# Kernel tuning notes

Hardware: AMD Instinct MI355X
Metric: run time of the kernel (lower is better)

## Reference

```python
import jax, jax.numpy as jnp
import numpy as np

EPS = 1e-8


def eq_linear(z, weight, bias):
    # EqualisedLinear: runtime weight scale c = 1/sqrt(in_features)
    c = 1.0 / np.sqrt(weight.shape[1]).astype(np.float32)
    return z @ (weight * c).T + bias


def mod_conv(x, w_raw, s, demodulate):
    # w_raw: [out, in, k, k], s: [b, in]
    out_c, in_c, k, _ = w_raw.shape
    c = 1.0 / np.sqrt(in_c * k * k).astype(np.float32)
    wt = w_raw * c
    # per-sample modulated weights: [b, out, in, k, k]
    ws = wt[None] * s[:, None, :, None, None]
    if demodulate:
        sigma_inv = jax.lax.rsqrt(jnp.sum(ws * ws, axis=(2, 3, 4), keepdims=True) + EPS)
        ws = ws * sigma_inv
    def conv1(xi, wi):
        return jax.lax.conv_general_dilated(
            xi[None], wi, window_strides=(1, 1), padding='SAME',
            dimension_numbers=('NCHW', 'OIHW', 'NCHW'))[0]
    return jax.vmap(conv1)(x, ws)


def lrelu(v):
    return jax.nn.leaky_relu(v, 0.2)


def style_block(x, w, noise, style_w, style_b, conv_w, noise_scale, bias):
    s = eq_linear(w, style_w, style_b)
    x = mod_conv(x, conv_w, s, demodulate=True)
    x = x + noise_scale[None, :, None, None] * noise
    return lrelu(x + bias[None, :, None, None])


def to_rgb(x, w, style_w, style_b, conv_w, bias):
    s = eq_linear(w, style_w, style_b)
    x = mod_conv(x, conv_w, s, demodulate=False)
    return lrelu(x + bias[None, :, None, None])


def setup_inputs() -> dict:
    key = jax.random.key(0)
    ks = jax.random.split(key, 16)
    B, C, H, W = 16, 512, 64, 64
    D = 512
    OUT = 3
    return {
        'x': jax.random.normal(ks[0], (B, C, H, W), jnp.float32),
        'w': jax.random.normal(ks[1], (B, D), jnp.float32),
        'noise1': jax.random.normal(ks[2], (B, 1, H, W), jnp.float32),
        'noise2': jax.random.normal(ks[3], (B, 1, H, W), jnp.float32),
        'sb1_style_w': jax.random.normal(ks[4], (C, D), jnp.float32),
        'sb1_style_b': jnp.ones((C,), jnp.float32),
        'sb1_conv_w': jax.random.normal(ks[5], (C, C, 3, 3), jnp.float32),
        'sb1_noise_scale': 0.1 * jax.random.normal(ks[6], (1,), jnp.float32),
        'sb1_bias': 0.1 * jax.random.normal(ks[7], (C,), jnp.float32),
        'sb2_style_w': jax.random.normal(ks[8], (C, D), jnp.float32),
        'sb2_style_b': jnp.ones((C,), jnp.float32),
        'sb2_conv_w': jax.random.normal(ks[9], (C, C, 3, 3), jnp.float32),
        'sb2_noise_scale': 0.1 * jax.random.normal(ks[10], (1,), jnp.float32),
        'sb2_bias': 0.1 * jax.random.normal(ks[11], (C,), jnp.float32),
        'rgb_style_w': jax.random.normal(ks[12], (C, D), jnp.float32),
        'rgb_style_b': jnp.ones((C,), jnp.float32),
        'rgb_conv_w': jax.random.normal(ks[13], (OUT, C, 1, 1), jnp.float32),
        'rgb_bias': 0.1 * jax.random.normal(ks[14], (OUT,), jnp.float32),
    }


def reference(x, w, noise1, noise2,
              sb1_style_w, sb1_style_b, sb1_conv_w, sb1_noise_scale, sb1_bias,
              sb2_style_w, sb2_style_b, sb2_conv_w, sb2_noise_scale, sb2_bias,
              rgb_style_w, rgb_style_b, rgb_conv_w, rgb_bias):
    x = style_block(x, w, noise1, sb1_style_w, sb1_style_b, sb1_conv_w, sb1_noise_scale, sb1_bias)
    x = style_block(x, w, noise2, sb2_style_w, sb2_style_b, sb2_conv_w, sb2_noise_scale, sb2_bias)
    rgb = to_rgb(x, w, rgb_style_w, rgb_style_b, rgb_conv_w, rgb_bias)
    return (x, rgb)
```

## Files before the change

### kernel.cpp

```cpp
#include <hip/hip_runtime.h>
#include <hip/hip_bf16.h>

typedef float f32x4 __attribute__((ext_vector_type(4)));
typedef short short8 __attribute__((ext_vector_type(8)));

#define CC    512
#define PIX   4096
#define ROWB  4224
#define TILE6 25344
#define TILE4 16896

__device__ __forceinline__ unsigned short f2bf(float f){
    __hip_bfloat16 h = __float2bfloat16(f);
    return __builtin_bit_cast(unsigned short, h);
}
__device__ __forceinline__ unsigned pk2(float a, float b){
    return (unsigned)f2bf(a) | ((unsigned)f2bf(b) << 16);
}
__device__ __forceinline__ void mfma_bf16(f32x4& c, short8 a, short8 b){
    asm("v_mfma_f32_16x16x32_bf16 %0, %1, %2, %0" : "+v"(c) : "v"(a), "v"(b));
}
__device__ __forceinline__ void gl_lds16(const void* g, void* l){
    __builtin_amdgcn_global_load_lds(
        (const __attribute__((address_space(1))) unsigned int*)g,
        (__attribute__((address_space(3))) unsigned int*)l, 16, 0, 0);
}

__global__ void k_style3(const float* __restrict__ w,
                         const float* __restrict__ sw0, const float* __restrict__ sb0, float* __restrict__ o0,
                         const float* __restrict__ sw1, const float* __restrict__ sb1, float* __restrict__ o1,
                         const float* __restrict__ sw2, const float* __restrict__ sb2, float* __restrict__ o2){
    __shared__ float wl[512];
    const int b = blockIdx.x, l = blockIdx.y, tid = threadIdx.x;
    const float* sw = (l==0) ? sw0 : (l==1 ? sw1 : sw2);
    const float* sb = (l==0) ? sb0 : (l==1 ? sb1 : sb2);
    float* so       = (l==0) ? o0  : (l==1 ? o1  : o2);
    wl[tid]       = w[b*512 + tid];
    wl[tid + 256] = w[b*512 + 256 + tid];
    __syncthreads();
    const float c = 0.044194173824159216f;
    for (int cc = tid; cc < 512; cc += 256){
        const float4* row = (const float4*)(sw + cc*512);
        float acc = 0.f;
        #pragma unroll 4
        for (int dd = 0; dd < 128; ++dd){
            float4 v = row[dd];
            float4 wv = ((const float4*)wl)[dd];
            acc += v.x*wv.x + v.y*wv.y + v.z*wv.z + v.w*wv.w;
        }
        so[b*512 + cc] = acc * c + sb[cc];
    }
}

__global__ void k_w2(const float* __restrict__ cw1, const float* __restrict__ cw2,
                     float* __restrict__ w2_1, float* __restrict__ w2_2){
    int gid = blockIdx.x*256 + threadIdx.x;
    int layer = gid >> 18; int r = gid & 262143;
    const float* cw = layer ? cw2 : cw1;
    float* w2 = layer ? w2_2 : w2_1;
    const float c2 = 1.0f/4608.0f;
    const float* p = cw + r*9;
    float sum = 0.f;
    #pragma unroll
    for (int t=0;t<9;++t){ float v = p[t]; sum += v*v; }
    w2[r] = sum * c2;
}

__global__ void k_demod2(const float* __restrict__ w21, const float* __restrict__ w22,
                         const float* __restrict__ s1,  const float* __restrict__ s2,
                         float* __restrict__ d1, float* __restrict__ d2){
    __shared__ float s2l[512];
    const int b = blockIdx.x, l = blockIdx.y, o = threadIdx.x;
    const float* w2 = l ? w22 : w21;
    const float* s  = l ? s2  : s1;
    float* d        = l ? d2  : d1;
    float sv = s[b*512 + o]; s2l[o] = sv*sv;
    __syncthreads();
    const float4* row = (const float4*)(w2 + o*512);
    const float4* sq  = (const float4*)s2l;
    float acc = 0.f;
    #pragma unroll 4
    for (int i=0;i<128;++i){
        float4 a = row[i], bq = sq[i];
        acc += a.x*bq.x + a.y*bq.y + a.z*bq.z + a.w*bq.w;
    }
    d[b*512 + o] = rsqrtf(acc + 1e-8f);
}

__global__ void k_pack(const float* __restrict__ cw1, const float* __restrict__ cw2,
                       uint4* __restrict__ wpk1, uint4* __restrict__ wpk2){
    int gid = blockIdx.x*256 + threadIdx.x;
    int layer = (gid >= 294912);
    int r = layer ? gid - 294912 : gid;
    const float* cw = layer ? cw2 : cw1;
    uint4* dst = layer ? wpk2 : wpk1;
    int lane = r & 63;
    int ofr  = (r>>6) & 31;
    int cb   = (r>>11) & 15;
    int t    = r>>15;
    int o  = ofr*16 + (lane&15);
    int i0 = cb*32 + (lane>>4)*8;
    const float c = 0.014731391274719738f;
    const float* src = cw + (o*512 + i0)*9 + t;
    float f[8];
    #pragma unroll
    for (int j=0;j<8;++j) f[j] = src[j*9]*c;
    uint4 wv;
    wv.x = pk2(f[0],f[1]); wv.y = pk2(f[2],f[3]);
    wv.z = pk2(f[4],f[5]); wv.w = pk2(f[6],f[7]);
    dst[r] = wv;
}

__global__ void k_stage_g(const float* __restrict__ x, const float* __restrict__ s,
                          char* __restrict__ xpg){
    __shared__ float s_lds[512];
    const int tid = threadIdx.x;
    const int rb = blockIdx.x, b = blockIdx.y;
    const int r0 = rb*4;
    s_lds[tid]       = s[b*512 + tid];
    s_lds[tid + 256] = s[b*512 + 256 + tid];
    __syncthreads();
    const int scol   = tid & 63;
    const int schunk = (tid>>6) & 3;
    unsigned wcol = (unsigned)((scol+1)*64 + schunk*16);
    wcol ^= (unsigned)((((scol+1)>>1)&3)<<4);
    const float* xb = x + (size_t)b * (512*PIX);
    for (int cb=0; cb<16; ++cb){
        char* dst = xpg + ((size_t)((b*16 + rb)*16 + cb))*TILE6;
        float sv[8];
        #pragma unroll
        for (int j=0;j<8;++j) sv[j] = s_lds[cb*32 + schunk*8 + j];
        const float* srcbase = xb + (size_t)(cb*32 + schunk*8)*PIX + scol;
        #pragma unroll
        for (int row=0; row<6; ++row){
            int gr = r0 - 1 + row;
            uint4 wq = make_uint4(0u,0u,0u,0u);
            if (0 <= gr && gr < 64){
                const float* sp = srcbase + gr*64;
                float f0 = sp[0*PIX]*sv[0], f1 = sp[1*PIX]*sv[1];
                float f2 = sp[2*PIX]*sv[2], f3 = sp[3*PIX]*sv[3];
                float f4 = sp[4*PIX]*sv[4], f5 = sp[5*PIX]*sv[5];
                float f6 = sp[6*PIX]*sv[6], f7 = sp[7*PIX]*sv[7];
                wq.x = pk2(f0,f1); wq.y = pk2(f2,f3);
                wq.z = pk2(f4,f5); wq.w = pk2(f6,f7);
            }
            *(uint4*)(dst + row*ROWB + wcol) = wq;
        }
        if (tid < 48){
            int row = tid>>3; int hc = (tid&4) ? 65 : 0; int ck = tid&3;
            unsigned a = (unsigned)((row*66 + hc)*64 + ck*16);
            a ^= (unsigned)(((hc>>1)&3)<<4);
            *(uint4*)(dst + a) = make_uint4(0u,0u,0u,0u);
        }
    }
}

__global__ __launch_bounds__(256, 2)
void k_conv(const char* __restrict__ xpg, float* __restrict__ y,
            const unsigned short* __restrict__ wpk,
            const float* __restrict__ dmod, const float* __restrict__ noise,
            const float* __restrict__ nsp, const float* __restrict__ bias){
    __shared__ __align__(16) char smem[2*TILE4];
    char* xh0 = smem;
    char* xh1 = smem + TILE4;

    const int tid  = threadIdx.x;
    const int obp  = blockIdx.x;
    const int rb   = blockIdx.y;
    const int b    = blockIdx.z;
    const int r0   = rb*2;
    const int lane = tid & 63;
    const int wv   = tid >> 6;
    const int ln15 = lane & 15;
    const int hi   = lane >> 4;

    f32x4 acc[4][8];
    #pragma unroll
    for (int mi=0;mi<4;++mi)
        #pragma unroll
        for (int ni=0;ni<8;++ni) acc[mi][ni] = (f32x4)(0.f);

    unsigned bcol[3][4];
    #pragma unroll
    for (int dxi=0; dxi<3; ++dxi)
        #pragma unroll
        for (int ni=0; ni<4; ++ni){
            int xcol = ni*16 + ln15 + dxi;
            unsigned a = (unsigned)(xcol*64 + hi*16);
            a ^= (unsigned)(((xcol>>1)&3)<<4);
            bcol[dxi][ni] = a;
        }

    const char* tbase = xpg + ((size_t)((b*16 + (rb>>1))*16))*TILE6
                            + (size_t)(rb&1)*2*ROWB;
    auto stage = [&](int cb2, char* dstb){
        const char* src = tbase + (size_t)cb2*TILE6;
        #pragma unroll
        for (int k=0;k<4;++k)
            gl_lds16(src + (size_t)(tid + k*256)*16, dstb + (tid + k*256)*16);
        if (tid < 32)
            gl_lds16(src + (size_t)(1024 + tid)*16, dstb + (1024 + tid)*16);
    };

    stage(0, xh0);

    const short8* wpf = (const short8*)wpk + (size_t)(obp*16 + wv*4)*64 + lane;

    #pragma unroll 2
    for (int cb=0; cb<16; ++cb){
        __syncthreads();
        const short8* wp = wpf + (size_t)cb*(32*64);
        short8 Af[4];
        #pragma unroll
        for (int mi=0;mi<4;++mi) Af[mi] = wp[mi*64];
        if (cb+1 < 16) stage(cb+1, (cb&1) ? xh0 : xh1);
        const char* cur = (cb&1) ? xh1 : xh0;
        #pragma unroll
        for (int t=0; t<9; ++t){
            const int dxi = t%3;
            if (t > 0){
                #pragma unroll
                for (int mi=0;mi<4;++mi) Af[mi] = wp[(size_t)t*(16*32*64) + mi*64];
            }
            const char* rbase0 = cur + (t/3)*ROWB;
            const char* rbase1 = rbase0 + ROWB;
            short8 Bf[8];
            #pragma unroll
            for (int ni=0;ni<4;++ni) Bf[ni]   = *(const short8*)(rbase0 + bcol[dxi][ni]);
            #pragma unroll
            for (int ni=0;ni<4;++ni) Bf[4+ni] = *(const short8*)(rbase1 + bcol[dxi][ni]);
            #pragma unroll
            for (int ni=0;ni<8;++ni)
                #pragma unroll
                for (int mi=0;mi<4;++mi)
                    mfma_bf16(acc[mi][ni], Af[mi], Bf[ni]);
        }
    }

    const int obase = obp*256 + wv*64;
    const float nsv = nsp[0];
    const float* dgl = dmod + b*512 + obase;
    const float* bgl = bias + obase;
    float nz[8];
    #pragma unroll
    for (int ni=0;ni<8;++ni){
        int row = r0 + (ni>>2);
        nz[ni] = nsv * noise[b*PIX + row*64 + (ni&3)*16 + ln15];
    }
    float* yb = y + ((size_t)(b*512 + obase))*PIX;
    #pragma unroll
    for (int mi=0;mi<4;++mi){
        float dv[4], bv[4];
        #pragma unroll
        for (int r=0;r<4;++r){
            int ol = mi*16 + hi*4 + r;
            dv[r] = dgl[ol]; bv[r] = bgl[ol];
        }
        #pragma unroll
        for (int ni=0;ni<8;++ni){
            int row = r0 + (ni>>2);
            int col = (ni&3)*16 + ln15;
            #pragma unroll
            for (int r=0;r<4;++r){
                float v = acc[mi][ni][r]*dv[r] + nz[ni] + bv[r];
                v = fmaxf(v, 0.2f*v);
                yb[(size_t)(mi*16 + hi*4 + r)*PIX + row*64 + col] = v;
            }
        }
    }
}

__global__ void k_rgb(const float* __restrict__ x2, const float* __restrict__ srgb,
                      const float* __restrict__ cw, const float* __restrict__ bias,
                      float* __restrict__ out){
    __shared__ float4 wr[512];
    const int b = blockIdx.x, tid = threadIdx.x;
    const float c = 0.044194173824159216f;
    for (int cc = tid; cc < 512; cc += 256){
        float sc = srgb[b*512 + cc]*c;
        wr[cc] = make_float4(cw[cc]*sc, cw[512+cc]*sc, cw[1024+cc]*sc, 0.f);
    }
    __syncthreads();
    int px = blockIdx.y*256 + tid;
    const float* xp = x2 + (size_t)b*(512*PIX) + px;
    float a0=0.f, a1=0.f, a2=0.f;
    #pragma unroll 4
    for (int i=0;i<512;++i){
        float xv = xp[(size_t)i*PIX];
        float4 wv = wr[i];
        a0 += wv.x*xv; a1 += wv.y*xv; a2 += wv.z*xv;
    }
    a0 += bias[0]; a1 += bias[1]; a2 += bias[2];
    out[(size_t)(b*3+0)*PIX + px] = fmaxf(a0, 0.2f*a0);
    out[(size_t)(b*3+1)*PIX + px] = fmaxf(a1, 0.2f*a1);
    out[(size_t)(b*3+2)*PIX + px] = fmaxf(a2, 0.2f*a2);
}

extern "C" void kernel_launch(void* const* d_in, const int* in_sizes, int n_in,
                              void* d_out, int out_size, void* d_ws, size_t ws_size,
                              hipStream_t stream) {
    const float* x    = (const float*)d_in[0];
    const float* w    = (const float*)d_in[1];
    const float* n1   = (const float*)d_in[2];
    const float* n2   = (const float*)d_in[3];
    const float* s1w  = (const float*)d_in[4];
    const float* s1b  = (const float*)d_in[5];
    const float* c1w  = (const float*)d_in[6];
    const float* ns1  = (const float*)d_in[7];
    const float* b1   = (const float*)d_in[8];
    const float* s2w  = (const float*)d_in[9];
    const float* s2b  = (const float*)d_in[10];
    const float* c2w  = (const float*)d_in[11];
    const float* ns2  = (const float*)d_in[12];
    const float* b2   = (const float*)d_in[13];
    const float* rw   = (const float*)d_in[14];
    const float* rbv  = (const float*)d_in[15];
    const float* rcw  = (const float*)d_in[16];
    const float* rbias= (const float*)d_in[17];

    float* out_x   = (float*)d_out;
    float* out_rgb = out_x + (size_t)16*512*PIX;

    char* ws = (char*)d_ws;
    float* s1   = (float*)(ws + 0);
    float* s2   = (float*)(ws + 32768);
    float* srgb = (float*)(ws + 65536);
    float* d1   = (float*)(ws + 98304);
    float* d2   = (float*)(ws + 131072);
    float* w21  = (float*)(ws + 163840);
    float* w22  = (float*)(ws + 163840 + 1048576);
    unsigned short* wp1 = (unsigned short*)(ws + 2260992);
    unsigned short* wp2 = wp1 + 2359296;
    char* xpg   = ws + 11698176;
    float* x1   = out_x;

    k_style3<<<dim3(16,3), 256, 0, stream>>>(w, s1w, s1b, s1, s2w, s2b, s2, rw, rbv, srgb);
    k_w2<<<2048, 256, 0, stream>>>(c1w, c2w, w21, w22);
    k_pack<<<2304, 256, 0, stream>>>(c1w, c2w, (uint4*)wp1, (uint4*)wp2);
    k_demod2<<<dim3(16,2), 512, 0, stream>>>(w21, w22, s1, s2, d1, d2);

    dim3 cg(2, 32, 16);
    k_stage_g<<<dim3(16,16), 256, 0, stream>>>(x, s1, xpg);
    k_conv<<<cg, 256, 0, stream>>>(xpg, x1, wp1, d1, n1, ns1, b1);
    k_stage_g<<<dim3(16,16), 256, 0, stream>>>(x1, s2, xpg);
    k_conv<<<cg, 256, 0, stream>>>(xpg, out_x, wp2, d2, n2, ns2, b2);
    k_rgb<<<dim3(16,16), 256, 0, stream>>>(out_x, srgb, rcw, rbias, out_rgb);
}
```

Baseline: 839.5 us.

## Reorder conv loop by input row to reuse B fragments; parallelize staging over channel blocks

The conv inner loop now iterates over the four staged input rows and loads each row's twelve B fragments once. It then applies them to both output rows using the matching weight taps, so LDS reads are no longer duplicated across the two output rows. In exchange, weight fragments are loaded per (row, tap, mi) inside the loop, and register pressure rises from holding twelve B fragments. Separately, the staging kernel now spreads channel blocks across a third grid dimension instead of looping serially, raising parallelism sixteen-fold.

```diff
diff --git a/kernel.cpp b/kernel.cpp
--- a/kernel.cpp
+++ b/kernel.cpp
@@ -113,45 +113,39 @@
 
 __global__ void k_stage_g(const float* __restrict__ x, const float* __restrict__ s,
                           char* __restrict__ xpg){
-    __shared__ float s_lds[512];
     const int tid = threadIdx.x;
-    const int rb = blockIdx.x, b = blockIdx.y;
+    const int cb = blockIdx.x, rb = blockIdx.y, b = blockIdx.z;
     const int r0 = rb*4;
-    s_lds[tid]       = s[b*512 + tid];
-    s_lds[tid + 256] = s[b*512 + 256 + tid];
-    __syncthreads();
     const int scol   = tid & 63;
     const int schunk = (tid>>6) & 3;
     unsigned wcol = (unsigned)((scol+1)*64 + schunk*16);
     wcol ^= (unsigned)((((scol+1)>>1)&3)<<4);
-    const float* xb = x + (size_t)b * (512*PIX);
-    for (int cb=0; cb<16; ++cb){
-        char* dst = xpg + ((size_t)((b*16 + rb)*16 + cb))*TILE6;
-        float sv[8];
-        #pragma unroll
-        for (int j=0;j<8;++j) sv[j] = s_lds[cb*32 + schunk*8 + j];
-        const float* srcbase = xb + (size_t)(cb*32 + schunk*8)*PIX + scol;
-        #pragma unroll
-        for (int row=0; row<6; ++row){
-            int gr = r0 - 1 + row;
-            uint4 wq = make_uint4(0u,0u,0u,0u);
-            if (0 <= gr && gr < 64){
-                const float* sp = srcbase + gr*64;
-                float f0 = sp[0*PIX]*sv[0], f1 = sp[1*PIX]*sv[1];
-                float f2 = sp[2*PIX]*sv[2], f3 = sp[3*PIX]*sv[3];
-                float f4 = sp[4*PIX]*sv[4], f5 = sp[5*PIX]*sv[5];
-                float f6 = sp[6*PIX]*sv[6], f7 = sp[7*PIX]*sv[7];
-                wq.x = pk2(f0,f1); wq.y = pk2(f2,f3);
-                wq.z = pk2(f4,f5); wq.w = pk2(f6,f7);
-            }
-            *(uint4*)(dst + row*ROWB + wcol) = wq;
-        }
-        if (tid < 48){
-            int row = tid>>3; int hc = (tid&4) ? 65 : 0; int ck = tid&3;
-            unsigned a = (unsigned)((row*66 + hc)*64 + ck*16);
-            a ^= (unsigned)(((hc>>1)&3)<<4);
-            *(uint4*)(dst + a) = make_uint4(0u,0u,0u,0u);
-        }
+    float sv[8];
+    const float* sp8 = s + b*512 + cb*32 + schunk*8;
+    #pragma unroll
+    for (int j=0;j<8;++j) sv[j] = sp8[j];
+    char* dst = xpg + ((size_t)((b*16 + rb)*16 + cb))*TILE6;
+    const float* srcbase = x + (size_t)b*(512*PIX) + (size_t)(cb*32 + schunk*8)*PIX + scol;
+    #pragma unroll
+    for (int row=0; row<6; ++row){
+        int gr = r0 - 1 + row;
+        uint4 wq = make_uint4(0u,0u,0u,0u);
+        if (0 <= gr && gr < 64){
+            const float* sp = srcbase + gr*64;
+            float f0 = sp[0*PIX]*sv[0], f1 = sp[1*PIX]*sv[1];
+            float f2 = sp[2*PIX]*sv[2], f3 = sp[3*PIX]*sv[3];
+            float f4 = sp[4*PIX]*sv[4], f5 = sp[5*PIX]*sv[5];
+            float f6 = sp[6*PIX]*sv[6], f7 = sp[7*PIX]*sv[7];
+            wq.x = pk2(f0,f1); wq.y = pk2(f2,f3);
+            wq.z = pk2(f4,f5); wq.w = pk2(f6,f7);
+        }
+        *(uint4*)(dst + row*ROWB + wcol) = wq;
+    }
+    if (tid < 48){
+        int row = tid>>3; int hc = (tid&4) ? 65 : 0; int ck = tid&3;
+        unsigned a = (unsigned)((row*66 + hc)*64 + ck*16);
+        a ^= (unsigned)(((hc>>1)&3)<<4);
+        *(uint4*)(dst + a) = make_uint4(0u,0u,0u,0u);
     }
 }
 
@@ -209,31 +203,36 @@
     #pragma unroll 2
     for (int cb=0; cb<16; ++cb){
         __syncthreads();
+        const char* cur = (cb&1) ? xh1 : xh0;
         const short8* wp = wpf + (size_t)cb*(32*64);
-        short8 Af[4];
-        #pragma unroll
-        for (int mi=0;mi<4;++mi) Af[mi] = wp[mi*64];
-        if (cb+1 < 16) stage(cb+1, (cb&1) ? xh0 : xh1);
-        const char* cur = (cb&1) ? xh1 : xh0;
-        #pragma unroll
-        for (int t=0; t<9; ++t){
-            const int dxi = t%3;
-            if (t > 0){
+        #pragma unroll
+        for (int ir=0; ir<4; ++ir){
+            short8 B[12];
+            const char* rbase = cur + ir*ROWB;
+            #pragma unroll
+            for (int dxi=0; dxi<3; ++dxi)
                 #pragma unroll
-                for (int mi=0;mi<4;++mi) Af[mi] = wp[(size_t)t*(16*32*64) + mi*64];
+                for (int ni=0; ni<4; ++ni)
+                    B[dxi*4+ni] = *(const short8*)(rbase + bcol[dxi][ni]);
+            #pragma unroll
+            for (int dxi=0; dxi<3; ++dxi){
+                #pragma unroll
+                for (int mi=0; mi<4; ++mi){
+                    if (ir < 3){
+                        short8 a0 = wp[(size_t)(ir*3+dxi)*(16*32*64) + mi*64];
+                        #pragma unroll
+                        for (int ni=0; ni<4; ++ni)
+                            mfma_bf16(acc[mi][ni], a0, B[dxi*4+ni]);
+                    }
+                    if (ir > 0){
+                        short8 a1 = wp[(size_t)((ir-1)*3+dxi)*(16*32*64) + mi*64];
+                        #pragma unroll
+                        for (int ni=0; ni<4; ++ni)
+                            mfma_bf16(acc[mi][4+ni], a1, B[dxi*4+ni]);
+                    }
+                }
             }
-            const char* rbase0 = cur + (t/3)*ROWB;
-            const char* rbase1 = rbase0 + ROWB;
-            short8 Bf[8];
-            #pragma unroll
-            for (int ni=0;ni<4;++ni) Bf[ni]   = *(const short8*)(rbase0 + bcol[dxi][ni]);
-            #pragma unroll
-            for (int ni=0;ni<4;++ni) Bf[4+ni] = *(const short8*)(rbase1 + bcol[dxi][ni]);
-            #pragma unroll
-            for (int ni=0;ni<8;++ni)
-                #pragma unroll
-                for (int mi=0;mi<4;++mi)
-                    mfma_bf16(acc[mi][ni], Af[mi], Bf[ni]);
+            if (ir == 0 && cb+1 < 16) stage(cb+1, (cb&1) ? xh0 : xh1);
         }
     }
 
@@ -340,9 +339,9 @@
     k_demod2<<<dim3(16,2), 512, 0, stream>>>(w21, w22, s1, s2, d1, d2);
 
     dim3 cg(2, 32, 16);
-    k_stage_g<<<dim3(16,16), 256, 0, stream>>>(x, s1, xpg);
+    k_stage_g<<<dim3(16,16,16), 256, 0, stream>>>(x, s1, xpg);
     k_conv<<<cg, 256, 0, stream>>>(xpg, x1, wp1, d1, n1, ns1, b1);
-    k_stage_g<<<dim3(16,16), 256, 0, stream>>>(x1, s2, xpg);
+    k_stage_g<<<dim3(16,16,16), 256, 0, stream>>>(x1, s2, xpg);
     k_conv<<<cg, 256, 0, stream>>>(xpg, out_x, wp2, d2, n2, ns2, b2);
     k_rgb<<<dim3(16,16), 256, 0, stream>>>(out_x, srgb, rcw, rbias, out_rgb);
 }
```

Measured after the change: 835.1 us. Within noise of the previous version (-0.5%).
